# Optimization experiments

Measured on AMD Instinct MI355X. Metric: run time of the kernel, lower is better.

The kernel has to match this reference:

```python
import jax, jax.numpy as jnp
import numpy as np

N, E, D = 50000, 800000, 256   # nodes, edges, hidden_dim
H, B, A = 8, 4, 3              # num_heads, num_bases, num_aggregators (symnorm,sum,max)
F = D // H                      # per-head width = bases feature width
G = 64                          # number of graphs in the batch
EPS = 1e-5                      # GraphNorm eps


def setup_inputs() -> dict:
    key = jax.random.key(0)
    ks = jax.random.split(key, 8)
    glorot = lambda k, shape: jax.random.normal(k, shape, jnp.float32) * np.sqrt(2.0 / (shape[0] + shape[1])).astype(np.float32)
    return {
        "node": jax.random.normal(ks[0], (N, D), jnp.float32),
        "edge_attr": jax.random.normal(ks[1], (E, 1), jnp.float32),  # unused by layer, kept for signature fidelity
        "W_bases": glorot(ks[2], (D, B * F)),                 # EGConv bases linear (no bias)
        "W_comb": glorot(ks[3], (D, H * B * A)),              # EGConv combination-weight linear
        "b_comb": jnp.zeros((H * B * A,), jnp.float32),
        "conv_bias": jnp.zeros((D,), jnp.float32),
        "gn_weight": jnp.ones((D,), jnp.float32),             # GraphNorm gamma
        "gn_bias": jnp.zeros((D,), jnp.float32),              # GraphNorm beta
        "gn_mean_scale": jnp.ones((D,), jnp.float32),         # GraphNorm alpha
        "edge_index": jax.random.randint(ks[4], (2, E), 0, N, dtype=jnp.int32),
        "batch": jnp.sort(jax.random.randint(ks[5], (N,), 0, G, dtype=jnp.int32)),
    }


def _forward(node, W_bases, W_comb, b_comb, conv_bias, gn_weight, gn_bias, gn_mean_scale, edge_index, batch):
    n = node.shape[0]
    loops = jnp.arange(n, dtype=edge_index.dtype)
    src = jnp.concatenate([edge_index[0], loops])  # add self-loops (EGConv add_self_loops=True / gcn_norm)
    dst = jnp.concatenate([edge_index[1], loops])

    # gcn_norm symmetric weights deg^-1/2[src] * deg^-1/2[dst]
    deg = jax.ops.segment_sum(jnp.ones_like(src, dtype=node.dtype), dst, num_segments=n)
    dinv = jnp.where(deg > 0, jax.lax.rsqrt(deg), 0.0)
    sym_w = dinv[src] * dinv[dst]

    bases = node @ W_bases            # [N, B*F]
    comb = node @ W_comb + b_comb     # [N, H*B*A]

    msg = bases[src]                  # [E+N, B*F] edge gather (dominant traffic)
    agg_sym = jax.ops.segment_sum(msg * sym_w[:, None], dst, num_segments=n)
    agg_sum = jax.ops.segment_sum(msg, dst, num_segments=n)
    agg_max = jax.ops.segment_max(msg, dst, num_segments=n)  # self-loops guarantee non-empty segments

    aggregated = jnp.stack([agg_sym, agg_sum, agg_max], axis=1)       # [N, A, B*F]
    aggregated = aggregated.reshape(n, A * B, F)                      # (a,b) fused index, as in PyG view
    weightings = comb.reshape(n, H, B * A)
    h = jnp.einsum('nhk,nkf->nhf', weightings, aggregated).reshape(n, D) + conv_bias

    # GraphNorm: per-graph mean/var with learnable mean scale alpha
    counts = jnp.maximum(jax.ops.segment_sum(jnp.ones((n,), node.dtype), batch, num_segments=G), 1.0)
    mean = jax.ops.segment_sum(h, batch, num_segments=G) / counts[:, None]
    hc = h - gn_mean_scale * mean[batch]
    var = jax.ops.segment_sum(hc * hc, batch, num_segments=G) / counts[:, None]
    out = gn_weight * hc * jax.lax.rsqrt(var[batch] + EPS) + gn_bias
    return jax.nn.relu(out)


def reference(node, edge_attr, W_bases, W_comb, b_comb, conv_bias, gn_weight, gn_bias, gn_mean_scale, edge_index, batch):
    del edge_attr  # unused by EGConv_layer, present in the torch forward signature
    return _forward(node, W_bases, W_comb, b_comb, conv_bias, gn_weight, gn_bias, gn_mean_scale, edge_index, batch)
```

## Files before the change

kernel.cpp:

```cpp
#include <hip/hip_runtime.h>
#include <hip/hip_bf16.h>

#define NN 50000
#define EE 800000
#define DD 256
#define BF 128
#define HC 96
#define GG 64
#define NT 14
#define KCN 8
#define NB 49
#define RS 3125
#define RC 16
#define CS 12500
#define CC 64
#define SL 8

typedef short s16x8 __attribute__((ext_vector_type(8)));
typedef float f32x4 __attribute__((ext_vector_type(4)));

static __device__ __forceinline__ float b2f(unsigned u) {
    unsigned x = u << 16;
    float f;
    __builtin_memcpy(&f, &x, 4);
    return f;
}
static __device__ __forceinline__ unsigned short f2b(float f) {
    unsigned x;
    __builtin_memcpy(&x, &f, 4);
    unsigned lsb = (x >> 16) & 1u;
    x += 0x7fffu + lsb;
    return (unsigned short)(x >> 16);
}
static __device__ __forceinline__ unsigned pack_trunc(float lo, float hi) {
    unsigned ulo, uhi;
    __builtin_memcpy(&ulo, &lo, 4);
    __builtin_memcpy(&uhi, &hi, 4);
    return (ulo >> 16) | (uhi & 0xffff0000u);
}

__global__ void k_setup(const unsigned short* node_u16, int* flag,
                        const void* bcomb, const void* cbias, const void* gw,
                        const void* gb, const void* gms,
                        float* bcombF, float* cbiasF, float* gwF, float* gbF, float* gmsF,
                        const int* batch, int* goff) {
    if (blockIdx.x == 0) {
        __shared__ int cnt;
        if (threadIdx.x == 0) cnt = 0;
        __syncthreads();
        int local = 0;
        #pragma unroll
        for (int j = 0; j < 4; j++) {
            int idx = 2 * (threadIdx.x * 4 + j);
            unsigned short u = node_u16[idx];
            int e = (u >> 7) & 0xFF;
            if (e < 100 || e > 140) local++;
        }
        atomicAdd(&cnt, local);
        __syncthreads();
        int isf = (cnt > 256) ? 1 : 0;
        if (threadIdx.x == 0) flag[0] = isf;
        int d = threadIdx.x;
        auto rd = [&](const void* p, int i) -> float {
            return isf ? ((const float*)p)[i] : b2f(((const unsigned short*)p)[i]);
        };
        if (d < HC) bcombF[d] = rd(bcomb, d);
        cbiasF[d] = rd(cbias, d);
        gwF[d] = rd(gw, d);
        gbF[d] = rd(gb, d);
        gmsF[d] = rd(gms, d);
    } else {
        int g = threadIdx.x;
        if (g > GG) return;
        int lo = 0, hi = NN;
        while (lo < hi) { int mid = (lo + hi) >> 1; if (batch[mid] < g) lo = mid + 1; else hi = mid; }
        goff[g] = lo;
    }
}

__global__ __launch_bounds__(256) void k_ehist(const int* ei, int* partial) {
    __shared__ int hist[RS];
    int c = blockIdx.x, r = blockIdx.y;
    for (int i = threadIdx.x; i < RS; i += 256) hist[i] = 0;
    __syncthreads();
    int base = r * RS;
    const int* dstp = ei + EE + (size_t)c * CS;
    for (int i = threadIdx.x; i < CS; i += 256) {
        int d = dstp[i] - base;
        if ((unsigned)d < RS) atomicAdd(&hist[d], 1);
    }
    __syncthreads();
    int* o = partial + (size_t)c * NN + base;
    for (int i = threadIdx.x; i < RS; i += 256) o[i] = hist[i];
}

__global__ void k_colscan(int* partial, int* deg) {
    int n = blockIdx.x * 256 + threadIdx.x;
    if (n >= NN) return;
    int run = 0;
    for (int c = 0; c < CC; c++) {
        size_t idx = (size_t)c * NN + n;
        int v = partial[idx];
        partial[idx] = run;
        run += v;
    }
    deg[n] = run + 1;
}

__global__ void k_scan1(const int* deg, int* bsum) {
    __shared__ int lds[256];
    int b = blockIdx.x, t = threadIdx.x;
    int base = b * 1024 + t * 4;
    int s = 0;
    #pragma unroll
    for (int j = 0; j < 4; j++) { int idx = base + j; if (idx < NN) s += deg[idx]; }
    lds[t] = s; __syncthreads();
    for (int ofs = 128; ofs > 0; ofs >>= 1) {
        if (t < ofs) lds[t] += lds[t + ofs];
        __syncthreads();
    }
    if (t == 0) bsum[b] = lds[0];
}

__global__ void k_scan2(const int* bsum, int* bpre, int* row_off) {
    if (threadIdx.x == 0) {
        int r = 0;
        for (int i = 0; i < NB; i++) { bpre[i] = r; r += bsum[i]; }
        row_off[NN] = r;
    }
}

__global__ void k_scan3(const int* deg, const int* bpre, int* row_off, float* dinv, int* csr) {
    __shared__ int lds[256];
    int b = blockIdx.x, t = threadIdx.x;
    int base = b * 1024 + t * 4;
    int d[4]; int s = 0;
    #pragma unroll
    for (int j = 0; j < 4; j++) { int idx = base + j; d[j] = (idx < NN) ? deg[idx] : 0; s += d[j]; }
    lds[t] = s; __syncthreads();
    for (int ofs = 1; ofs < 256; ofs <<= 1) {
        int add = (t >= ofs) ? lds[t - ofs] : 0;
        __syncthreads();
        lds[t] += add;
        __syncthreads();
    }
    int excl = lds[t] - s + bpre[b];
    #pragma unroll
    for (int j = 0; j < 4; j++) {
        int idx = base + j;
        if (idx < NN) {
            row_off[idx] = excl;
            csr[excl] = idx;
            excl += d[j];
            dinv[idx] = rsqrtf((float)deg[idx]);
        }
    }
}

__global__ __launch_bounds__(256) void k_escatter(const int* ei, const int* row_off,
                                                  const int* partial, int* csr) {
    __shared__ int cur[RS];
    int c = blockIdx.x, r = blockIdx.y;
    int base = r * RS;
    const int* po = partial + (size_t)c * NN + base;
    const int* ro = row_off + base;
    for (int i = threadIdx.x; i < RS; i += 256) cur[i] = ro[i] + 1 + po[i];
    __syncthreads();
    const int* srcp = ei + (size_t)c * CS;
    const int* dstp = ei + EE + (size_t)c * CS;
    for (int i = threadIdx.x; i < CS; i += 256) {
        int d = dstp[i] - base;
        int s = srcp[i];
        if ((unsigned)d < RS) {
            int slot = atomicAdd(&cur[d], 1);
            csr[slot] = s;
        }
    }
}

__global__ void k_pack(const int* flag, const void* Wb, const void* Wc, unsigned short* wpack) {
    int t = blockIdx.x, kc = blockIdx.y, lane = threadIdx.x;
    int isf = flag[0];
    int n = t * 16 + (lane & 15);
    int kb = kc * 32 + (lane >> 4) * 8;
    unsigned short* o = wpack + (size_t)(((t * KCN) + kc) * 64 + lane) * 8;
    #pragma unroll
    for (int j = 0; j < 8; j++) {
        int k = kb + j;
        int src = (n < BF) ? (k * BF + n) : (k * HC + (n - BF));
        const void* W = (n < BF) ? Wb : Wc;
        o[j] = isf ? f2b(((const float*)W)[src]) : ((const unsigned short*)W)[src];
    }
}

__global__ __launch_bounds__(256) void k_gemm(const int* flag, const void* node,
                                              const unsigned short* wpack, const float* bcombF,
                                              unsigned short* bases, float* comb) {
    int wv = threadIdx.x >> 6, lane = threadIdx.x & 63;
    int row0 = blockIdx.x * 64 + wv * 16;
    int m = row0 + (lane & 15);
    int mc = m < NN ? m : NN - 1;
    int kg = lane >> 4;
    int isf = flag[0];
    const s16x8* bp = reinterpret_cast<const s16x8*>(wpack);
    f32x4 acc[NT];
    #pragma unroll
    for (int t = 0; t < NT; t++) acc[t] = (f32x4){0.f, 0.f, 0.f, 0.f};
    if (isf) {
        const float* nf = (const float*)node + (size_t)mc * DD;
        for (int kc = 0; kc < KCN; kc++) {
            const f32x4* src = reinterpret_cast<const f32x4*>(nf + kc * 32 + kg * 8);
            f32x4 x0 = src[0], x1 = src[1];
            union { s16x8 v; unsigned u[4]; } a;
            a.u[0] = pack_trunc(x0[0], x0[1]);
            a.u[1] = pack_trunc(x0[2], x0[3]);
            a.u[2] = pack_trunc(x1[0], x1[1]);
            a.u[3] = pack_trunc(x1[2], x1[3]);
            #pragma unroll
            for (int t = 0; t < NT; t++) {
                s16x8 b = bp[(size_t)(t * KCN + kc) * 64 + lane];
                acc[t] = __builtin_amdgcn_mfma_f32_16x16x32_bf16(a.v, b, acc[t], 0, 0, 0);
            }
        }
    } else {
        const s16x8* ap = reinterpret_cast<const s16x8*>(node);
        for (int kc = 0; kc < KCN; kc++) {
            s16x8 a = ap[(size_t)mc * 32 + kc * 4 + kg];
            #pragma unroll
            for (int t = 0; t < NT; t++) {
                s16x8 b = bp[(size_t)(t * KCN + kc) * 64 + lane];
                acc[t] = __builtin_amdgcn_mfma_f32_16x16x32_bf16(a, b, acc[t], 0, 0, 0);
            }
        }
    }
    int colb = lane & 15;
    #pragma unroll
    for (int t = 0; t < NT; t++) {
        int nc = t * 16 + colb;
        #pragma unroll
        for (int i = 0; i < 4; i++) {
            int r = row0 + kg * 4 + i;
            if (r < NN) {
                float v = acc[t][i];
                if (nc < BF) bases[(size_t)r * BF + nc] = f2b(v);
                else comb[(size_t)r * HC + (nc - BF)] = v + bcombF[nc - BF];
            }
        }
    }
}

__global__ __launch_bounds__(256) void k_agg(const unsigned short* bases,
                                             const float* comb, const float* dinv,
                                             const int* row_off, const int* csr,
                                             const float* cbiasF, unsigned short* h) {
    __shared__ float2 lds[4][3][64];
    int wv = threadIdx.x >> 6, lane = threadIdx.x & 63;
    int v = blockIdx.x * 4 + wv;
    int r0 = row_off[v], r1 = row_off[v + 1];
    float dv = dinv[v];
    const unsigned* bp = reinterpret_cast<const unsigned*>(bases);
    float sy0 = 0.f, sy1 = 0.f, su0 = 0.f, su1 = 0.f;
    float mx0 = -3.4e38f, mx1 = -3.4e38f;
    for (int base = r0; base < r1; base += 64) {
        int nload = r1 - base; if (nload > 64) nload = 64;
        int sidx = 0; float wgt = 0.f;
        if (lane < nload) { sidx = csr[base + lane]; wgt = dinv[sidx] * dv; }
        int j = 0;
        for (; j + 4 <= nload; j += 4) {
            int s0 = __shfl(sidx, j),     s1 = __shfl(sidx, j + 1);
            int s2 = __shfl(sidx, j + 2), s3 = __shfl(sidx, j + 3);
            float w0 = __shfl(wgt, j),     w1 = __shfl(wgt, j + 1);
            float w2 = __shfl(wgt, j + 2), w3 = __shfl(wgt, j + 3);
            unsigned g0 = bp[(size_t)s0 * 64 + lane];
            unsigned g1 = bp[(size_t)s1 * 64 + lane];
            unsigned g2 = bp[(size_t)s2 * 64 + lane];
            unsigned g3 = bp[(size_t)s3 * 64 + lane];
            float a, b;
            a = b2f(g0 & 0xffffu); b = b2f(g0 >> 16);
            sy0 += w0 * a; sy1 += w0 * b; su0 += a; su1 += b; mx0 = fmaxf(mx0, a); mx1 = fmaxf(mx1, b);
            a = b2f(g1 & 0xffffu); b = b2f(g1 >> 16);
            sy0 += w1 * a; sy1 += w1 * b; su0 += a; su1 += b; mx0 = fmaxf(mx0, a); mx1 = fmaxf(mx1, b);
            a = b2f(g2 & 0xffffu); b = b2f(g2 >> 16);
            sy0 += w2 * a; sy1 += w2 * b; su0 += a; su1 += b; mx0 = fmaxf(mx0, a); mx1 = fmaxf(mx1, b);
            a = b2f(g3 & 0xffffu); b = b2f(g3 >> 16);
            sy0 += w3 * a; sy1 += w3 * b; su0 += a; su1 += b; mx0 = fmaxf(mx0, a); mx1 = fmaxf(mx1, b);
        }
        for (; j < nload; j++) {
            int s0 = __shfl(sidx, j); float w0 = __shfl(wgt, j);
            unsigned g0 = bp[(size_t)s0 * 64 + lane];
            float a = b2f(g0 & 0xffffu), b = b2f(g0 >> 16);
            sy0 += w0 * a; sy1 += w0 * b; su0 += a; su1 += b; mx0 = fmaxf(mx0, a); mx1 = fmaxf(mx1, b);
        }
    }
    lds[wv][0][lane] = (float2){sy0, sy1};
    lds[wv][1][lane] = (float2){su0, su1};
    lds[wv][2][lane] = (float2){mx0, mx1};
    __syncthreads();
    const float* P0 = (const float*)&lds[wv][0][0];
    const float* P1 = (const float*)&lds[wv][1][0];
    const float* P2 = (const float*)&lds[wv][2][0];
    int d0 = lane * 4;
    int hh = d0 >> 5;
    float cb[12];
    #pragma unroll
    for (int k = 0; k < 12; k++) cb[k] = comb[(size_t)v * HC + hh * 12 + k];
    union { unsigned short e[4]; uint2 u; } o;
    #pragma unroll
    for (int i = 0; i < 4; i++) {
        int d = d0 + i, f = d & 31;
        float acc = cbiasF[d];
        #pragma unroll
        for (int k = 0; k < 12; k++) {
            int a = k >> 2, b = k & 3;
            const float* P = (a == 0) ? P0 : ((a == 1) ? P1 : P2);
            acc += cb[k] * P[b * 32 + f];
        }
        o.e[i] = f2b(acc);
    }
    reinterpret_cast<uint2*>(h)[(size_t)v * 64 + lane] = o.u;
}

__global__ void k_stats1(const unsigned short* h, const int* goff, float* sstat) {
    int g = blockIdx.x, s = blockIdx.y, t = threadIdx.x;
    int v0 = goff[g], v1 = goff[g + 1];
    float sum = 0.f, sq = 0.f;
    for (int v = v0 + s; v < v1; v += SL) {
        float x = b2f(h[(size_t)v * DD + t]);
        sum += x; sq += x * x;
    }
    size_t o = ((size_t)(g * SL + s)) * (2 * DD);
    sstat[o + t] = sum;
    sstat[o + DD + t] = sq;
}

__global__ void k_stats2(const float* sstat, const int* goff,
                         const float* gwF, const float* gbF, const float* gmsF,
                         float* sA, float* sB) {
    int g = blockIdx.x, d = threadIdx.x;
    float sum = 0.f, sq = 0.f;
    #pragma unroll
    for (int s = 0; s < SL; s++) {
        size_t o = ((size_t)(g * SL + s)) * (2 * DD);
        sum += sstat[o + d];
        sq  += sstat[o + DD + d];
    }
    int c = goff[g + 1] - goff[g];
    float cnt = (float)(c > 1 ? c : 1);
    float mu = sum / cnt;
    float m2 = sq / cnt;
    float al = gmsF[d];
    float var = m2 - mu * mu * (2.f * al - al * al);
    float rstd = rsqrtf(var + 1e-5f);
    float sa = gwF[d] * rstd;
    sA[g * DD + d] = sa;
    sB[g * DD + d] = gbF[d] - sa * al * mu;
}

__global__ void k_out(const int* flag, const unsigned short* h, const int* batch,
                      const float* sA, const float* sB, void* out) {
    int tid = blockIdx.x * 256 + threadIdx.x;
    int v = tid >> 6, q = tid & 63;
    if (v >= NN) return;
    int g = batch[v];
    uint2 xr = reinterpret_cast<const uint2*>(h)[(size_t)v * 64 + q];
    f32x4 a = reinterpret_cast<const f32x4*>(sA)[g * 64 + q];
    f32x4 b = reinterpret_cast<const f32x4*>(sB)[g * 64 + q];
    float x0 = b2f(xr.x & 0xffffu), x1 = b2f(xr.x >> 16);
    float x2 = b2f(xr.y & 0xffffu), x3 = b2f(xr.y >> 16);
    float y0 = fmaxf(x0 * a[0] + b[0], 0.f);
    float y1 = fmaxf(x1 * a[1] + b[1], 0.f);
    float y2 = fmaxf(x2 * a[2] + b[2], 0.f);
    float y3 = fmaxf(x3 * a[3] + b[3], 0.f);
    if (flag[0]) {
        f32x4 y = {y0, y1, y2, y3};
        reinterpret_cast<f32x4*>(out)[(size_t)v * 64 + q] = y;
    } else {
        union { unsigned short e[4]; uint2 u; } o;
        o.e[0] = f2b(y0); o.e[1] = f2b(y1); o.e[2] = f2b(y2); o.e[3] = f2b(y3);
        reinterpret_cast<uint2*>(out)[(size_t)v * 64 + q] = o.u;
    }
}

extern "C" void kernel_launch(void* const* d_in, const int* in_sizes, int n_in,
                              void* d_out, int out_size, void* d_ws, size_t ws_size,
                              hipStream_t stream) {
    const void* node  = d_in[0];
    const void* Wb    = d_in[2];
    const void* Wc    = d_in[3];
    const void* bcomb = d_in[4];
    const void* cbias = d_in[5];
    const void* gw    = d_in[6];
    const void* gb    = d_in[7];
    const void* gms   = d_in[8];
    const int* ei     = (const int*)d_in[9];
    const int* batch  = (const int*)d_in[10];

    char* w = (char*)d_ws;
    size_t off = 0;
    auto alloc = [&](size_t bytes) -> void* {
        off = (off + 255) & ~(size_t)255;
        void* p = w + off;
        off += bytes;
        return p;
    };
    unsigned short* bases = (unsigned short*)alloc((size_t)NN * BF * 2);
    float* comb    = (float*)alloc((size_t)NN * HC * 4);
    unsigned short* h = (unsigned short*)alloc((size_t)NN * DD * 2);
    int*   csr     = (int*)alloc((size_t)(EE + NN) * 4);
    int*   partial = (int*)alloc((size_t)CC * NN * 4);
    int*   deg     = (int*)alloc((size_t)NN * 4);
    float* dinv    = (float*)alloc((size_t)NN * 4);
    int*   row_off = (int*)alloc((size_t)(NN + 1) * 4);
    int*   bsum    = (int*)alloc((size_t)NB * 4);
    int*   bpre    = (int*)alloc((size_t)NB * 4);
    int*   goff    = (int*)alloc((size_t)(GG + 1) * 4);
    float* sstat   = (float*)alloc((size_t)GG * SL * 2 * DD * 4);
    float* sA      = (float*)alloc((size_t)GG * DD * 4);
    float* sB      = (float*)alloc((size_t)GG * DD * 4);
    unsigned short* wpack = (unsigned short*)alloc((size_t)NT * KCN * 64 * 8 * 2);
    int*   flag    = (int*)alloc(256);
    float* bcombF  = (float*)alloc(HC * 4);
    float* cbiasF  = (float*)alloc(DD * 4);
    float* gwF     = (float*)alloc(DD * 4);
    float* gbF     = (float*)alloc(DD * 4);
    float* gmsF    = (float*)alloc(DD * 4);

    k_setup<<<2, 256, 0, stream>>>((const unsigned short*)node, flag, bcomb, cbias, gw, gb, gms,
                                   bcombF, cbiasF, gwF, gbF, gmsF, batch, goff);
    k_ehist<<<dim3(CC, RC), 256, 0, stream>>>(ei, partial);
    k_colscan<<<(NN + 255) / 256, 256, 0, stream>>>(partial, deg);
    k_scan1<<<NB, 256, 0, stream>>>(deg, bsum);
    k_scan2<<<1, 64, 0, stream>>>(bsum, bpre, row_off);
    k_scan3<<<NB, 256, 0, stream>>>(deg, bpre, row_off, dinv, csr);
    k_escatter<<<dim3(CC, RC), 256, 0, stream>>>(ei, row_off, partial, csr);
    k_pack<<<dim3(NT, KCN), 64, 0, stream>>>(flag, Wb, Wc, wpack);
    k_gemm<<<(NN + 63) / 64, 256, 0, stream>>>(flag, node, wpack, bcombF, bases, comb);
    k_agg<<<NN / 4, 256, 0, stream>>>(bases, comb, dinv, row_off, csr, cbiasF, h);
    k_stats1<<<dim3(GG, SL), 256, 0, stream>>>(h, goff, sstat);
    k_stats2<<<GG, 256, 0, stream>>>(sstat, goff, gwF, gbF, gmsF, sA, sB);
    k_out<<<(NN * 64 + 255) / 256, 256, 0, stream>>>(flag, h, batch, sA, sB, d_out);
}
```

Measured before the change: 313.1 us.

## Build CSR via two-level radix bucketing instead of dense partial histograms

Replaces the CSR construction, which used a 64x50000 partial histogram, a column scan and three scan kernels, with a coarse bucket sort. Edges are counted into 98 row-range buckets of 512 nodes each, scanned, and scattered as packed (src, local dst) words. Each bucket is then sorted locally in LDS to emit row offsets, dinv and CSR entries with self-loops. This cuts the large partial-array traffic, the repeated full passes over edges per row chunk, and the kernel count. It relies on a fixed per-bucket capacity (CAP=10240, stage 10752) that could overflow for skewed degree distributions.

Result: faster. 271.2 us (-13.4%).

```diff
diff --git a/kernel.cpp b/kernel.cpp
--- a/kernel.cpp
+++ b/kernel.cpp
@@ -9,12 +9,14 @@
 #define GG 64
 #define NT 14
 #define KCN 8
-#define NB 49
-#define RS 3125
-#define RC 16
-#define CS 12500
-#define CC 64
+#define RC 98
+#define RSH 9
+#define RSZ 512
+#define CC 256
+#define CS 3125
+#define CAP 10240
 #define SL 8
+#define STG 10752
 
 typedef short s16x8 __attribute__((ext_vector_type(8)));
 typedef float f32x4 __attribute__((ext_vector_type(4)));
@@ -78,104 +80,119 @@
     }
 }
 
-__global__ __launch_bounds__(256) void k_ehist(const int* ei, int* partial) {
-    __shared__ int hist[RS];
-    int c = blockIdx.x, r = blockIdx.y;
-    for (int i = threadIdx.x; i < RS; i += 256) hist[i] = 0;
-    __syncthreads();
-    int base = r * RS;
+__global__ __launch_bounds__(256) void k_cnt(const int* ei, int* cntg) {
+    __shared__ int cnt[RC];
+    int c = blockIdx.x, t = threadIdx.x;
+    if (t < RC) cnt[t] = 0;
+    __syncthreads();
     const int* dstp = ei + EE + (size_t)c * CS;
-    for (int i = threadIdx.x; i < CS; i += 256) {
-        int d = dstp[i] - base;
-        if ((unsigned)d < RS) atomicAdd(&hist[d], 1);
-    }
-    __syncthreads();
-    int* o = partial + (size_t)c * NN + base;
-    for (int i = threadIdx.x; i < RS; i += 256) o[i] = hist[i];
-}
-
-__global__ void k_colscan(int* partial, int* deg) {
-    int n = blockIdx.x * 256 + threadIdx.x;
-    if (n >= NN) return;
-    int run = 0;
-    for (int c = 0; c < CC; c++) {
-        size_t idx = (size_t)c * NN + n;
-        int v = partial[idx];
-        partial[idx] = run;
-        run += v;
-    }
-    deg[n] = run + 1;
-}
-
-__global__ void k_scan1(const int* deg, int* bsum) {
+    for (int i = t; i < CS; i += 256) atomicAdd(&cnt[dstp[i] >> RSH], 1);
+    __syncthreads();
+    if (t < RC) cntg[c * RC + t] = cnt[t];
+}
+
+__global__ __launch_bounds__(256) void k_cscan(const int* cntg, int* baseg, int* cntr) {
     __shared__ int lds[256];
-    int b = blockIdx.x, t = threadIdx.x;
-    int base = b * 1024 + t * 4;
-    int s = 0;
-    #pragma unroll
-    for (int j = 0; j < 4; j++) { int idx = base + j; if (idx < NN) s += deg[idx]; }
-    lds[t] = s; __syncthreads();
-    for (int ofs = 128; ofs > 0; ofs >>= 1) {
-        if (t < ofs) lds[t] += lds[t + ofs];
-        __syncthreads();
-    }
-    if (t == 0) bsum[b] = lds[0];
-}
-
-__global__ void k_scan2(const int* bsum, int* bpre, int* row_off) {
-    if (threadIdx.x == 0) {
-        int r = 0;
-        for (int i = 0; i < NB; i++) { bpre[i] = r; r += bsum[i]; }
-        row_off[NN] = r;
-    }
-}
-
-__global__ void k_scan3(const int* deg, const int* bpre, int* row_off, float* dinv, int* csr) {
-    __shared__ int lds[256];
-    int b = blockIdx.x, t = threadIdx.x;
-    int base = b * 1024 + t * 4;
-    int d[4]; int s = 0;
-    #pragma unroll
-    for (int j = 0; j < 4; j++) { int idx = base + j; d[j] = (idx < NN) ? deg[idx] : 0; s += d[j]; }
-    lds[t] = s; __syncthreads();
+    int r = blockIdx.x, t = threadIdx.x;
+    int v = cntg[t * RC + r];
+    lds[t] = v;
+    __syncthreads();
     for (int ofs = 1; ofs < 256; ofs <<= 1) {
         int add = (t >= ofs) ? lds[t - ofs] : 0;
         __syncthreads();
         lds[t] += add;
         __syncthreads();
     }
-    int excl = lds[t] - s + bpre[b];
-    #pragma unroll
-    for (int j = 0; j < 4; j++) {
-        int idx = base + j;
-        if (idx < NN) {
-            row_off[idx] = excl;
-            csr[excl] = idx;
-            excl += d[j];
-            dinv[idx] = rsqrtf((float)deg[idx]);
-        }
-    }
-}
-
-__global__ __launch_bounds__(256) void k_escatter(const int* ei, const int* row_off,
-                                                  const int* partial, int* csr) {
-    __shared__ int cur[RS];
-    int c = blockIdx.x, r = blockIdx.y;
-    int base = r * RS;
-    const int* po = partial + (size_t)c * NN + base;
-    const int* ro = row_off + base;
-    for (int i = threadIdx.x; i < RS; i += 256) cur[i] = ro[i] + 1 + po[i];
+    baseg[t * RC + r] = r * CAP + lds[t] - v;
+    if (t == 255) cntr[r] = lds[255];
+}
+
+__global__ void k_rscan(const int* cntr, int* rbase, int* row_off) {
+    __shared__ int lds[128];
+    int t = threadIdx.x;
+    int nr = (t < RC) ? ((t == RC - 1) ? (NN - (RC - 1) * RSZ) : RSZ) : 0;
+    int v = (t < RC) ? cntr[t] + nr : 0;
+    lds[t] = v;
+    __syncthreads();
+    for (int ofs = 1; ofs < 128; ofs <<= 1) {
+        int add = (t >= ofs) ? lds[t - ofs] : 0;
+        __syncthreads();
+        lds[t] += add;
+        __syncthreads();
+    }
+    if (t < RC) rbase[t] = lds[t] - v;
+    if (t == RC - 1) row_off[NN] = lds[t];
+}
+
+__global__ __launch_bounds__(256) void k_bucket(const int* ei, const int* baseg, unsigned* bucket) {
+    __shared__ int cur[RC];
+    int c = blockIdx.x, t = threadIdx.x;
+    if (t < RC) cur[t] = baseg[c * RC + t];
     __syncthreads();
     const int* srcp = ei + (size_t)c * CS;
     const int* dstp = ei + EE + (size_t)c * CS;
-    for (int i = threadIdx.x; i < CS; i += 256) {
-        int d = dstp[i] - base;
-        int s = srcp[i];
-        if ((unsigned)d < RS) {
-            int slot = atomicAdd(&cur[d], 1);
-            csr[slot] = s;
-        }
-    }
+    for (int i = t; i < CS; i += 256) {
+        int d = dstp[i], s = srcp[i];
+        int r = d >> RSH;
+        int pos = atomicAdd(&cur[r], 1);
+        bucket[pos] = ((unsigned)s << RSH) | (unsigned)(d & (RSZ - 1));
+    }
+}
+
+__global__ __launch_bounds__(256) void k_build(const unsigned* bucket, const int* cntr,
+                                               const int* rbase, int* row_off, float* dinv,
+                                               int* csr) {
+    __shared__ int hist[RSZ];
+    __shared__ int stage[STG];
+    __shared__ int scanbuf[256];
+    int r = blockIdx.x, t = threadIdx.x;
+    int n0 = r * RSZ;
+    int nr = NN - n0; if (nr > RSZ) nr = RSZ;
+    int cr = cntr[r];
+    int rb = rbase[r];
+    const unsigned* bk = bucket + (size_t)r * CAP;
+    #pragma unroll
+    for (int j = 0; j < 2; j++) hist[t + j * 256] = 0;
+    __syncthreads();
+    for (int i = t; i < cr; i += 256) atomicAdd(&hist[bk[i] & (RSZ - 1)], 1);
+    __syncthreads();
+    int a0 = (2 * t     < nr) ? hist[2 * t] + 1     : 0;
+    int a1 = (2 * t + 1 < nr) ? hist[2 * t + 1] + 1 : 0;
+    int s = a0 + a1;
+    scanbuf[t] = s;
+    __syncthreads();
+    for (int ofs = 1; ofs < 256; ofs <<= 1) {
+        int add = (t >= ofs) ? scanbuf[t - ofs] : 0;
+        __syncthreads();
+        scanbuf[t] += add;
+        __syncthreads();
+    }
+    int excl = scanbuf[t] - s;
+    int total = scanbuf[255];
+    __syncthreads();
+    if (2 * t < nr) {
+        int n = 2 * t;
+        row_off[n0 + n] = rb + excl;
+        dinv[n0 + n] = rsqrtf((float)a0);
+        stage[excl] = n0 + n;
+        hist[n] = excl + 1;
+    }
+    if (2 * t + 1 < nr) {
+        int n = 2 * t + 1;
+        int e1 = excl + a0;
+        row_off[n0 + n] = rb + e1;
+        dinv[n0 + n] = rsqrtf((float)a1);
+        stage[e1] = n0 + n;
+        hist[n] = e1 + 1;
+    }
+    __syncthreads();
+    for (int i = t; i < cr; i += 256) {
+        unsigned p = bk[i];
+        int slot = atomicAdd(&hist[p & (RSZ - 1)], 1);
+        stage[slot] = (int)(p >> RSH);
+    }
+    __syncthreads();
+    for (int i = t; i < total; i += 256) csr[rb + i] = stage[i];
 }
 
 __global__ void k_pack(const int* flag, const void* Wb, const void* Wc, unsigned short* wpack) {
@@ -407,12 +424,13 @@
     float* comb    = (float*)alloc((size_t)NN * HC * 4);
     unsigned short* h = (unsigned short*)alloc((size_t)NN * DD * 2);
     int*   csr     = (int*)alloc((size_t)(EE + NN) * 4);
-    int*   partial = (int*)alloc((size_t)CC * NN * 4);
-    int*   deg     = (int*)alloc((size_t)NN * 4);
+    unsigned* bucket = (unsigned*)alloc((size_t)RC * CAP * 4);
+    int*   cntg    = (int*)alloc((size_t)CC * RC * 4);
+    int*   baseg   = (int*)alloc((size_t)CC * RC * 4);
+    int*   cntrr   = (int*)alloc((size_t)RC * 4);
+    int*   rbase   = (int*)alloc((size_t)RC * 4);
     float* dinv    = (float*)alloc((size_t)NN * 4);
     int*   row_off = (int*)alloc((size_t)(NN + 1) * 4);
-    int*   bsum    = (int*)alloc((size_t)NB * 4);
-    int*   bpre    = (int*)alloc((size_t)NB * 4);
     int*   goff    = (int*)alloc((size_t)(GG + 1) * 4);
     float* sstat   = (float*)alloc((size_t)GG * SL * 2 * DD * 4);
     float* sA      = (float*)alloc((size_t)GG * DD * 4);
@@ -427,12 +445,11 @@
 
     k_setup<<<2, 256, 0, stream>>>((const unsigned short*)node, flag, bcomb, cbias, gw, gb, gms,
                                    bcombF, cbiasF, gwF, gbF, gmsF, batch, goff);
-    k_ehist<<<dim3(CC, RC), 256, 0, stream>>>(ei, partial);
-    k_colscan<<<(NN + 255) / 256, 256, 0, stream>>>(partial, deg);
-    k_scan1<<<NB, 256, 0, stream>>>(deg, bsum);
-    k_scan2<<<1, 64, 0, stream>>>(bsum, bpre, row_off);
-    k_scan3<<<NB, 256, 0, stream>>>(deg, bpre, row_off, dinv, csr);
-    k_escatter<<<dim3(CC, RC), 256, 0, stream>>>(ei, row_off, partial, csr);
+    k_cnt<<<CC, 256, 0, stream>>>(ei, cntg);
+    k_cscan<<<RC, 256, 0, stream>>>(cntg, baseg, cntrr);
+    k_rscan<<<1, 128, 0, stream>>>(cntrr, rbase, row_off);
+    k_bucket<<<CC, 256, 0, stream>>>(ei, baseg, bucket);
+    k_build<<<RC, 256, 0, stream>>>(bucket, cntrr, rbase, row_off, dinv, csr);
     k_pack<<<dim3(NT, KCN), 64, 0, stream>>>(flag, Wb, Wc, wpack);
     k_gemm<<<(NN + 63) / 64, 256, 0, stream>>>(flag, node, wpack, bcombF, bases, comb);
     k_agg<<<NN / 4, 256, 0, stream>>>(bases, comb, dinv, row_off, csr, cbiasF, h);
```
